# Kernel optimization log

Measured on AMD Instinct MI355X. Metric: run time of the kernel, lower is better.

The kernel has to match this reference:

```python
import jax, jax.numpy as jnp
import numpy as np

IN_DIM = 128
OUT_DIM = 128
SPLINE_ORDER = 3
GRID_SIZE = 5
NUM_BASIS = GRID_SIZE + SPLINE_ORDER  # 8


def _make_grid():
    # linspace(-1, 1, grid_size+1) extended by spline_order knots on each side
    steps = GRID_SIZE + 1
    g = np.linspace(-1.0, 1.0, steps, dtype=np.float32)
    h = (g[-1] - g[0]) / (steps - 1)
    for _ in range(SPLINE_ORDER):
        g = np.concatenate([[g[0] - h], g, [g[-1] + h]])
    # expand to [in_dim, G]
    return jnp.asarray(np.broadcast_to(g, (IN_DIM, g.shape[0])).copy())


def setup_inputs() -> dict:
    key = jax.random.key(0)
    kx, kc, kw = jax.random.split(key, 3)
    x = jax.random.normal(kx, (8192, IN_DIM), dtype=jnp.float32)
    grid = _make_grid()                                                  # [in, 12]
    spline_coeff = jax.random.normal(kc, (IN_DIM, OUT_DIM, NUM_BASIS), dtype=jnp.float32)
    base_weight = jax.random.normal(kw, (IN_DIM, OUT_DIM), dtype=jnp.float32)
    scale = jnp.ones((1,), dtype=jnp.float32)
    return {"x": x, "grid": grid, "spline_coeff": spline_coeff,
            "base_weight": base_weight, "scale": scale}


def _b_spline_basis(x, grid, order):
    # x: [B, in]; grid: [in, G] -> basis [B, in, G-1-order]
    xg = x[:, :, None]            # [B, in, 1]
    g = grid[None, :, :]          # [1, in, G]
    basis = ((xg >= g[:, :, :-1]) & (xg < g[:, :, 1:])).astype(x.dtype)
    basis = jnp.nan_to_num(basis)
    for k in range(1, order + 1):
        left = (xg - g[:, :, :-(k + 1)]) / (g[:, :, k:-1] - g[:, :, :-(k + 1)]) * basis[:, :, :-1]
        right = (g[:, :, k + 1:] - xg) / (g[:, :, k + 1:] - g[:, :, 1:-k]) * basis[:, :, 1:]
        basis = jnp.nan_to_num(left + right)
    return basis


def reference(x, grid, spline_coeff, base_weight, scale):
    silu = jax.nn.silu(x)                                   # [B, in]
    basis = _b_spline_basis(x, grid, SPLINE_ORDER)          # [B, in, num_basis]
    spline = jnp.einsum('bij,ikj->bik', basis, spline_coeff)  # [B, in, out]
    base = silu[:, :, None] * base_weight[None, :, :]       # [B, in, out]
    y = (base + spline) * scale
    return y.sum(axis=1)                                    # [B, out]
```

## Files before the change

### kernel.cpp

```cpp
#include <hip/hip_runtime.h>
#include <hip/hip_bf16.h>
#include <cstdint>
#include <cstddef>

#define IN_DIM 128
#define OUT_DIM 128
#define NB 8
#define KDIM 1152
#define BM 32
#define NT 9
#define B_TILE_BYTES (128 * 256)
#define A_ROW_BYTES 2304
#define A_BYTES (BM * A_ROW_BYTES)

using bf16 = __hip_bfloat16;
typedef __attribute__((ext_vector_type(8))) short short8;
typedef __attribute__((ext_vector_type(4))) float f32x4;

__device__ __forceinline__ void basis_weights(float xv, float g0, float inv_h,
                                              int& j, float& w0, float& w1,
                                              float& w2, float& w3) {
    float t = (xv - g0) * inv_h;
    float jf = floorf(t);
    j = (int)jf;
    float u = t - jf;
    float um = 1.f - u;
    float u2 = u * u, u3 = u2 * u;
    w0 = um * um * um * (1.f / 6.f);
    w1 = (3.f * u3 - 6.f * u2 + 4.f) * (1.f / 6.f);
    w2 = (-3.f * u3 + 3.f * u2 + 3.f * u + 1.f) * (1.f / 6.f);
    w3 = u3 * (1.f / 6.f);
}

__device__ __forceinline__ unsigned short to_bf16_bits(float v) {
    bf16 h = __float2bfloat16(v);
    return *(unsigned short*)&h;
}

__global__ __launch_bounds__(512)
void k_kan(const float* __restrict__ x, const float* __restrict__ grid,
           const float* __restrict__ C, const float* __restrict__ W,
           const float* __restrict__ scale, float* __restrict__ out) {
    __shared__ __align__(16) char smem[A_BYTES + 2 * B_TILE_BYTES];
    char* Abase = smem;
    char* Bbase = smem + A_BYTES;

    const int tid = threadIdx.x;
    const int lane = tid & 63;
    const int m0 = blockIdx.x * BM;

#pragma unroll
    for (int inst = 0; inst < 4; ++inst) {
        int c = inst * 512 + tid;
        int o = c & 127, ch = c >> 7;
        const float* src = C + ((size_t)ch * 128 + o) * 8;
        float4 va = *(const float4*)src;
        float4 vb = *(const float4*)(src + 4);
        short8 pk;
        pk[0] = (short)to_bf16_bits(va.x); pk[1] = (short)to_bf16_bits(va.y);
        pk[2] = (short)to_bf16_bits(va.z); pk[3] = (short)to_bf16_bits(va.w);
        pk[4] = (short)to_bf16_bits(vb.x); pk[5] = (short)to_bf16_bits(vb.y);
        pk[6] = (short)to_bf16_bits(vb.z); pk[7] = (short)to_bf16_bits(vb.w);
        *(short8*)(Bbase + o * 256 + ((ch ^ (o & 7)) << 4)) = pk;
    }

    {
        int row = tid >> 4, ip = tid & 15;
        const float* xr = x + (size_t)(m0 + row) * IN_DIM + ip * 8;
        float4 xa = *(const float4*)xr;
        float4 xb = *(const float4*)(xr + 4);
        float xv[8] = {xa.x, xa.y, xa.z, xa.w, xb.x, xb.y, xb.z, xb.w};
        float g0 = grid[0];
        float inv_h = 1.f / (grid[4] - grid[3]);
        char* Arow = Abase + row * A_ROW_BYTES;
        short8 sil;
#pragma unroll
        for (int e = 0; e < 8; ++e) {
            float v = xv[e];
            sil[e] = (short)to_bf16_bits(v / (1.f + __expf(-v)));
            int j; float w0, w1, w2, w3;
            basis_weights(v, g0, inv_h, j, w0, w1, w2, w3);
            bool inr = (j >= 0) && (j < 11);
            short8 bas;
#pragma unroll
            for (int m = 0; m < 8; ++m) {
                int k2 = m - (j - 3);
                float val = 0.f;
                if (inr && k2 >= 0 && k2 < 4)
                    val = (k2 == 0) ? w0 : (k2 == 1) ? w1 : (k2 == 2) ? w2 : w3;
                bas[m] = (short)to_bf16_bits(val);
            }
            int chunk = (ip * 8 + e) ^ (row & 7);
            *(short8*)(Arow + chunk * 16) = bas;
        }
        int chunk = (128 + ip) ^ (row & 7);
        *(short8*)(Arow + chunk * 16) = sil;
    }
    __syncthreads();

    const int w = (tid >> 6) & 3, g = tid >> 8;
    const int r0 = lane & 15;
    const int ksub = lane >> 4;
    f32x4 acc[2][2];
#pragma unroll
    for (int rg = 0; rg < 2; ++rg)
#pragma unroll
        for (int n = 0; n < 2; ++n) acc[rg][n] = 0.f;

    int cur = 0;
    for (int t = 0; t < NT; ++t) {
        float4 st[4][2];
        const bool do_stage = (t + 1 < NT);
        if (do_stage) {
            if (t + 1 < 8) {
                int i0 = (t + 1) * 16;
#pragma unroll
                for (int inst = 0; inst < 4; ++inst) {
                    int c = inst * 512 + tid;
                    int o = c & 127, ch = c >> 7;
                    const float* src = C + ((size_t)(i0 + ch) * 128 + o) * 8;
                    st[inst][0] = *(const float4*)src;
                    st[inst][1] = *(const float4*)(src + 4);
                }
            } else {
#pragma unroll
                for (int inst = 0; inst < 4; ++inst) {
                    int c = inst * 512 + tid;
                    int o = c & 127, ch = c >> 7;
                    float v[8];
#pragma unroll
                    for (int s = 0; s < 8; ++s)
                        v[s] = W[(size_t)(ch * 8 + s) * 128 + o];
                    st[inst][0] = make_float4(v[0], v[1], v[2], v[3]);
                    st[inst][1] = make_float4(v[4], v[5], v[6], v[7]);
                }
            }
        }

        const char* Bbuf = Bbase + cur * B_TILE_BYTES;
        short8 a[2][2], b[2][2];
#pragma unroll
        for (int rg = 0; rg < 2; ++rg) {
            int row = rg * 16 + r0;
#pragma unroll
            for (int k2 = 0; k2 < 2; ++k2) {
                int c = t * 16 + (g * 2 + k2) * 4 + ksub;
                int cs = c ^ (row & 7);
                a[rg][k2] = *(const short8*)(Abase + row * A_ROW_BYTES + cs * 16);
            }
        }
#pragma unroll
        for (int n = 0; n < 2; ++n) {
            int o = w * 32 + n * 16 + r0;
#pragma unroll
            for (int k2 = 0; k2 < 2; ++k2) {
                int ch = (g * 2 + k2) * 4 + ksub;
                b[n][k2] = *(const short8*)(Bbuf + o * 256 + ((ch ^ (o & 7)) << 4));
            }
        }
#pragma unroll
        for (int k2 = 0; k2 < 2; ++k2)
#pragma unroll
            for (int rg = 0; rg < 2; ++rg)
#pragma unroll
                for (int n = 0; n < 2; ++n)
                    acc[rg][n] = __builtin_amdgcn_mfma_f32_16x16x32_bf16(
                        a[rg][k2], b[n][k2], acc[rg][n], 0, 0, 0);

        if (do_stage) {
            char* Bnxt = Bbase + (cur ^ 1) * B_TILE_BYTES;
#pragma unroll
            for (int inst = 0; inst < 4; ++inst) {
                int c = inst * 512 + tid;
                int o = c & 127, ch = c >> 7;
                short8 pk;
                pk[0] = (short)to_bf16_bits(st[inst][0].x);
                pk[1] = (short)to_bf16_bits(st[inst][0].y);
                pk[2] = (short)to_bf16_bits(st[inst][0].z);
                pk[3] = (short)to_bf16_bits(st[inst][0].w);
                pk[4] = (short)to_bf16_bits(st[inst][1].x);
                pk[5] = (short)to_bf16_bits(st[inst][1].y);
                pk[6] = (short)to_bf16_bits(st[inst][1].z);
                pk[7] = (short)to_bf16_bits(st[inst][1].w);
                *(short8*)(Bnxt + o * 256 + ((ch ^ (o & 7)) << 4)) = pk;
            }
        }
        __syncthreads();
        cur ^= 1;
    }

    float* pane = (float*)smem;
    const int pbase = w * (32 * 33);
    if (g == 1) {
#pragma unroll
        for (int rg = 0; rg < 2; ++rg)
#pragma unroll
            for (int n = 0; n < 2; ++n)
#pragma unroll
                for (int q = 0; q < 4; ++q) {
                    int row = rg * 16 + ksub * 4 + q;
                    pane[pbase + row * 33 + n * 16 + r0] = acc[rg][n][q];
                }
    }
    __syncthreads();
    if (g == 0) {
        float s = scale[0];
#pragma unroll
        for (int rg = 0; rg < 2; ++rg)
#pragma unroll
            for (int n = 0; n < 2; ++n)
#pragma unroll
                for (int q = 0; q < 4; ++q) {
                    int row = rg * 16 + ksub * 4 + q;
                    float v = acc[rg][n][q] + pane[pbase + row * 33 + n * 16 + r0];
                    out[(size_t)(m0 + row) * OUT_DIM + w * 32 + n * 16 + r0] = v * s;
                }
    }
}

__global__ void k_naive(const float* __restrict__ x, const float* __restrict__ grid,
                        const float* __restrict__ C, const float* __restrict__ W,
                        const float* __restrict__ scale, float* __restrict__ out) {
    __shared__ float sS[128];
    __shared__ float sB[128][8];
    int b = blockIdx.x, t = threadIdx.x;
    float xv = x[(size_t)b * IN_DIM + t];
    float g0 = grid[0];
    float inv_h = 1.f / (grid[4] - grid[3]);
    sS[t] = xv / (1.f + __expf(-xv));
    int j; float w0, w1, w2, w3;
    basis_weights(xv, g0, inv_h, j, w0, w1, w2, w3);
    bool inrange = (j >= 0) && (j < 11);
#pragma unroll
    for (int m = 0; m < 8; ++m) {
        int k2 = m - (j - 3);
        float val = 0.f;
        if (inrange && k2 >= 0 && k2 < 4)
            val = (k2 == 0) ? w0 : (k2 == 1) ? w1 : (k2 == 2) ? w2 : w3;
        sB[t][m] = val;
    }
    __syncthreads();
    float acc = 0.f;
    for (int i = 0; i < IN_DIM; ++i) {
        acc += sS[i] * W[(size_t)i * OUT_DIM + t];
        const float* c = C + ((size_t)i * OUT_DIM + t) * NB;
#pragma unroll
        for (int m = 0; m < 8; ++m) acc += sB[i][m] * c[m];
    }
    out[(size_t)b * OUT_DIM + t] = acc * scale[0];
}

extern "C" void kernel_launch(void* const* d_in, const int* in_sizes, int n_in,
                              void* d_out, int out_size, void* d_ws, size_t ws_size,
                              hipStream_t stream) {
    const float* x     = (const float*)d_in[0];
    const float* grid  = (const float*)d_in[1];
    const float* C     = (const float*)d_in[2];
    const float* W     = (const float*)d_in[3];
    const float* scale = (const float*)d_in[4];
    float* out = (float*)d_out;

    int B = in_sizes[0] / IN_DIM;

    if ((B % BM) == 0) {
        k_kan<<<B / BM, 512, 0, stream>>>(x, grid, C, W, scale, out);
    } else {
        k_naive<<<B, 128, 0, stream>>>(x, grid, C, W, scale, out);
    }
}
```

Measured before the change: 18.05 us.

## Load B operands directly from global into registers, drop LDS staging

Each wave now loads its own spline-coefficient and base-weight fragments from global memory into registers, with a one-tile register prefetch, and converts them to bf16 just before the MFMAs. This removes the shared-memory B double buffer and the per-tile __syncthreads, shrinking LDS use to the A tile. In exchange, B data is fetched redundantly by each of the 4 row groups per block and by every block, the base-weight loads stay strided, and register pressure rises.

```diff
diff --git a/kernel.cpp b/kernel.cpp
--- a/kernel.cpp
+++ b/kernel.cpp
@@ -6,10 +6,8 @@
 #define IN_DIM 128
 #define OUT_DIM 128
 #define NB 8
-#define KDIM 1152
 #define BM 32
 #define NT 9
-#define B_TILE_BYTES (128 * 256)
 #define A_ROW_BYTES 2304
 #define A_BYTES (BM * A_ROW_BYTES)
 
@@ -37,32 +35,65 @@
     return *(unsigned short*)&h;
 }
 
+__device__ __forceinline__ short8 pack8(const float4& a, const float4& b) {
+    short8 p;
+    p[0] = (short)to_bf16_bits(a.x); p[1] = (short)to_bf16_bits(a.y);
+    p[2] = (short)to_bf16_bits(a.z); p[3] = (short)to_bf16_bits(a.w);
+    p[4] = (short)to_bf16_bits(b.x); p[5] = (short)to_bf16_bits(b.y);
+    p[6] = (short)to_bf16_bits(b.z); p[7] = (short)to_bf16_bits(b.w);
+    return p;
+}
+
 __global__ __launch_bounds__(512)
 void k_kan(const float* __restrict__ x, const float* __restrict__ grid,
            const float* __restrict__ C, const float* __restrict__ W,
            const float* __restrict__ scale, float* __restrict__ out) {
-    __shared__ __align__(16) char smem[A_BYTES + 2 * B_TILE_BYTES];
-    char* Abase = smem;
-    char* Bbase = smem + A_BYTES;
+    __shared__ __align__(16) char smem[A_BYTES];
 
     const int tid = threadIdx.x;
     const int lane = tid & 63;
     const int m0 = blockIdx.x * BM;
-
-#pragma unroll
-    for (int inst = 0; inst < 4; ++inst) {
-        int c = inst * 512 + tid;
-        int o = c & 127, ch = c >> 7;
-        const float* src = C + ((size_t)ch * 128 + o) * 8;
-        float4 va = *(const float4*)src;
-        float4 vb = *(const float4*)(src + 4);
-        short8 pk;
-        pk[0] = (short)to_bf16_bits(va.x); pk[1] = (short)to_bf16_bits(va.y);
-        pk[2] = (short)to_bf16_bits(va.z); pk[3] = (short)to_bf16_bits(va.w);
-        pk[4] = (short)to_bf16_bits(vb.x); pk[5] = (short)to_bf16_bits(vb.y);
-        pk[6] = (short)to_bf16_bits(vb.z); pk[7] = (short)to_bf16_bits(vb.w);
-        *(short8*)(Bbase + o * 256 + ((ch ^ (o & 7)) << 4)) = pk;
-    }
+    const int w = (tid >> 6) & 3;
+    const int g = tid >> 8;
+    const int r0 = lane & 15;
+    const int ksub = lane >> 4;
+
+    int ocol[2];
+    ocol[0] = w * 32 + r0;
+    ocol[1] = w * 32 + 16 + r0;
+
+    float4 cb[2][2][2];
+    float4 pf[2][2][2];
+
+    auto load_spline = [&](int t, float4 (&dst)[2][2][2]) {
+#pragma unroll
+        for (int k2 = 0; k2 < 2; ++k2) {
+            int i = t * 16 + (2 * g + k2) * 4 + ksub;
+#pragma unroll
+            for (int n = 0; n < 2; ++n) {
+                const float* src = C + ((size_t)i * 128 + ocol[n]) * 8;
+                dst[k2][n][0] = *(const float4*)src;
+                dst[k2][n][1] = *(const float4*)(src + 4);
+            }
+        }
+    };
+    auto load_base = [&](float4 (&dst)[2][2][2]) {
+#pragma unroll
+        for (int k2 = 0; k2 < 2; ++k2) {
+            int ibase = (2 * g + k2) * 32 + ksub * 8;
+#pragma unroll
+            for (int n = 0; n < 2; ++n) {
+                float v[8];
+#pragma unroll
+                for (int e = 0; e < 8; ++e)
+                    v[e] = W[(size_t)(ibase + e) * 128 + ocol[n]];
+                dst[k2][n][0] = make_float4(v[0], v[1], v[2], v[3]);
+                dst[k2][n][1] = make_float4(v[4], v[5], v[6], v[7]);
+            }
+        }
+    };
+
+    load_spline(0, cb);
 
     {
         int row = tid >> 4, ip = tid & 15;
@@ -72,7 +103,7 @@
         float xv[8] = {xa.x, xa.y, xa.z, xa.w, xb.x, xb.y, xb.z, xb.w};
         float g0 = grid[0];
         float inv_h = 1.f / (grid[4] - grid[3]);
-        char* Arow = Abase + row * A_ROW_BYTES;
+        char* Arow = smem + row * A_ROW_BYTES;
         short8 sil;
 #pragma unroll
         for (int e = 0; e < 8; ++e) {
@@ -98,64 +129,33 @@
     }
     __syncthreads();
 
-    const int w = (tid >> 6) & 3, g = tid >> 8;
-    const int r0 = lane & 15;
-    const int ksub = lane >> 4;
     f32x4 acc[2][2];
 #pragma unroll
     for (int rg = 0; rg < 2; ++rg)
 #pragma unroll
         for (int n = 0; n < 2; ++n) acc[rg][n] = 0.f;
 
-    int cur = 0;
+#pragma unroll
     for (int t = 0; t < NT; ++t) {
-        float4 st[4][2];
-        const bool do_stage = (t + 1 < NT);
-        if (do_stage) {
-            if (t + 1 < 8) {
-                int i0 = (t + 1) * 16;
-#pragma unroll
-                for (int inst = 0; inst < 4; ++inst) {
-                    int c = inst * 512 + tid;
-                    int o = c & 127, ch = c >> 7;
-                    const float* src = C + ((size_t)(i0 + ch) * 128 + o) * 8;
-                    st[inst][0] = *(const float4*)src;
-                    st[inst][1] = *(const float4*)(src + 4);
-                }
-            } else {
-#pragma unroll
-                for (int inst = 0; inst < 4; ++inst) {
-                    int c = inst * 512 + tid;
-                    int o = c & 127, ch = c >> 7;
-                    float v[8];
-#pragma unroll
-                    for (int s = 0; s < 8; ++s)
-                        v[s] = W[(size_t)(ch * 8 + s) * 128 + o];
-                    st[inst][0] = make_float4(v[0], v[1], v[2], v[3]);
-                    st[inst][1] = make_float4(v[4], v[5], v[6], v[7]);
-                }
-            }
-        }
-
-        const char* Bbuf = Bbase + cur * B_TILE_BYTES;
-        short8 a[2][2], b[2][2];
+        if (t + 1 < 8)        load_spline(t + 1, pf);
+        else if (t + 1 == 8)  load_base(pf);
+
+        short8 b[2][2];
+#pragma unroll
+        for (int k2 = 0; k2 < 2; ++k2)
+#pragma unroll
+            for (int n = 0; n < 2; ++n)
+                b[k2][n] = pack8(cb[k2][n][0], cb[k2][n][1]);
+
+        short8 a[2][2];
 #pragma unroll
         for (int rg = 0; rg < 2; ++rg) {
             int row = rg * 16 + r0;
 #pragma unroll
             for (int k2 = 0; k2 < 2; ++k2) {
-                int c = t * 16 + (g * 2 + k2) * 4 + ksub;
+                int c = t * 16 + (2 * g + k2) * 4 + ksub;
                 int cs = c ^ (row & 7);
-                a[rg][k2] = *(const short8*)(Abase + row * A_ROW_BYTES + cs * 16);
-            }
-        }
-#pragma unroll
-        for (int n = 0; n < 2; ++n) {
-            int o = w * 32 + n * 16 + r0;
-#pragma unroll
-            for (int k2 = 0; k2 < 2; ++k2) {
-                int ch = (g * 2 + k2) * 4 + ksub;
-                b[n][k2] = *(const short8*)(Bbuf + o * 256 + ((ch ^ (o & 7)) << 4));
+                a[rg][k2] = *(const short8*)(smem + row * A_ROW_BYTES + cs * 16);
             }
         }
 #pragma unroll
@@ -165,30 +165,20 @@
 #pragma unroll
                 for (int n = 0; n < 2; ++n)
                     acc[rg][n] = __builtin_amdgcn_mfma_f32_16x16x32_bf16(
-                        a[rg][k2], b[n][k2], acc[rg][n], 0, 0, 0);
-
-        if (do_stage) {
-            char* Bnxt = Bbase + (cur ^ 1) * B_TILE_BYTES;
-#pragma unroll
-            for (int inst = 0; inst < 4; ++inst) {
-                int c = inst * 512 + tid;
-                int o = c & 127, ch = c >> 7;
-                short8 pk;
-                pk[0] = (short)to_bf16_bits(st[inst][0].x);
-                pk[1] = (short)to_bf16_bits(st[inst][0].y);
-                pk[2] = (short)to_bf16_bits(st[inst][0].z);
-                pk[3] = (short)to_bf16_bits(st[inst][0].w);
-                pk[4] = (short)to_bf16_bits(st[inst][1].x);
-                pk[5] = (short)to_bf16_bits(st[inst][1].y);
-                pk[6] = (short)to_bf16_bits(st[inst][1].z);
-                pk[7] = (short)to_bf16_bits(st[inst][1].w);
-                *(short8*)(Bnxt + o * 256 + ((ch ^ (o & 7)) << 4)) = pk;
-            }
-        }
-        __syncthreads();
-        cur ^= 1;
-    }
-
+                        a[rg][k2], b[k2][n], acc[rg][n], 0, 0, 0);
+
+        if (t + 1 < NT) {
+#pragma unroll
+            for (int k2 = 0; k2 < 2; ++k2)
+#pragma unroll
+                for (int n = 0; n < 2; ++n)
+#pragma unroll
+                    for (int h = 0; h < 2; ++h)
+                        cb[k2][n][h] = pf[k2][n][h];
+        }
+    }
+
+    __syncthreads();
     float* pane = (float*)smem;
     const int pbase = w * (32 * 33);
     if (g == 1) {
```

Result: faster. 16.35 us (-9.4%).
